# Kernel tuning notes

Hardware: AMD Instinct MI355X
Metric: run time of the kernel (lower is better)

The kernel has to match this reference:

```python
import jax, jax.numpy as jnp
import numpy as np

D_OUT, D_IN, R, N_TOK = 4096, 4096, 16, 8192

def setup_inputs() -> dict:
    key = jax.random.key(0)
    k1, k2, k3, k4 = jax.random.split(key, 4)
    x = jax.random.normal(k1, (N_TOK, D_IN), dtype=jnp.float32)
    W = jax.random.normal(k2, (D_OUT, D_IN), dtype=jnp.float32) * (1.0 / np.sqrt(D_IN))
    bias = jax.random.normal(k3, (D_OUT,), dtype=jnp.float32) * 0.02
    lora_B = jnp.zeros((D_OUT, R), dtype=jnp.float32)  # torch init: zeros
    lora_A = jax.random.normal(k4, (R, D_IN), dtype=jnp.float32) / R  # torch init: randn / r
    lora_scale = jnp.float32(1.0)
    return {"x": x, "W": W, "bias": bias, "lora_B": lora_B, "lora_A": lora_A, "lora_scale": lora_scale}

def reference(x, W, bias, lora_B, lora_A, lora_scale):
    # Faithful to torch: weight = W + scale * B @ A; out = x @ weight.T + bias
    weight = W + lora_scale * (lora_B @ lora_A)  # [d_out, d_in]
    return jnp.einsum('ni,oi->no', x, weight) + bias
```

## Files before the change

kernel.cpp:

```cpp
#include <hip/hip_runtime.h>
#include <stdint.h>
#include <stddef.h>

#define M_TOK 8192
#define N_OUT 4096
#define K_IN  4096
#define R_LORA 16

#define BM 256
#define BN 256
#define BK 64
#define NT (K_IN / BK)

#define WEFF_BLOCKS ((K_IN / 1024) * (N_OUT / 16))
#define CAST_BLOCKS ((M_TOK * K_IN) / (8 * 256))

typedef __bf16 bf16_t;
typedef __bf16 bf16x4 __attribute__((ext_vector_type(4)));
typedef __bf16 bf16x8 __attribute__((ext_vector_type(8)));
typedef float floatx4 __attribute__((ext_vector_type(4)));

__device__ inline void async_copy16(const bf16_t* g, bf16_t* l) {
  __builtin_amdgcn_global_load_lds(
      (__attribute__((address_space(1))) void*)(uintptr_t)(const void*)g,
      (__attribute__((address_space(3))) void*)l,
      16, 0, 0);
}

#define BAR()   __builtin_amdgcn_s_barrier()
#define VMCNT4  asm volatile("s_waitcnt vmcnt(4)" ::: "memory")
#define VMCNT2  asm volatile("s_waitcnt vmcnt(2)" ::: "memory")
#define VMCNT0  asm volatile("s_waitcnt vmcnt(0)" ::: "memory")

__global__ __launch_bounds__(256) void prep_fused(
    const float* __restrict__ x, bf16_t* __restrict__ xb,
    const float* __restrict__ W, const float* __restrict__ lB,
    const float* __restrict__ lA, const float* __restrict__ scale_p,
    bf16_t* __restrict__ wb) {
  const int b = blockIdx.x;
  if (b < WEFF_BLOCKS) {
    const int kbase = (b & 3) * 1024 + threadIdx.x * 4;
    const int o0    = (b >> 2) * 16;
    const float scale = *scale_p;

    float4 areg[R_LORA];
#pragma unroll
    for (int r = 0; r < R_LORA; ++r)
      areg[r] = *(const float4*)(lA + (size_t)r * K_IN + kbase);

    for (int oo = 0; oo < 16; ++oo) {
      const int o = o0 + oo;
      float4 w = *(const float4*)(W + (size_t)o * K_IN + kbase);
      float a0 = w.x, a1 = w.y, a2 = w.z, a3 = w.w;
#pragma unroll
      for (int r = 0; r < R_LORA; ++r) {
        float bb = lB[(size_t)o * R_LORA + r] * scale;
        a0 += bb * areg[r].x; a1 += bb * areg[r].y;
        a2 += bb * areg[r].z; a3 += bb * areg[r].w;
      }
      bf16x4 v;
      v[0] = (bf16_t)a0; v[1] = (bf16_t)a1; v[2] = (bf16_t)a2; v[3] = (bf16_t)a3;
      *(bf16x4*)(wb + (size_t)o * K_IN + kbase) = v;
    }
  } else {
    const size_t t = (size_t)(b - WEFF_BLOCKS) * 256 + threadIdx.x;
    const float4* xp = (const float4*)x + t * 2;
    float4 a0 = xp[0];
    float4 a1 = xp[1];
    bf16x8 v;
    v[0] = (bf16_t)a0.x; v[1] = (bf16_t)a0.y; v[2] = (bf16_t)a0.z; v[3] = (bf16_t)a0.w;
    v[4] = (bf16_t)a1.x; v[5] = (bf16_t)a1.y; v[6] = (bf16_t)a1.z; v[7] = (bf16_t)a1.w;
    *(bf16x8*)(xb + t * 8) = v;
  }
}

__global__ __launch_bounds__(512, 2) void gemm_bt256(const bf16_t* __restrict__ A,
                                                     const bf16_t* __restrict__ Bw,
                                                     const float* __restrict__ bias,
                                                     float* __restrict__ C) {
  __shared__ bf16_t sA[2 * 2 * 128 * 64];
  __shared__ bf16_t sB[2 * 2 * 128 * 64];

  const int tid  = threadIdx.x;
  const int wave = tid >> 6;
  const int lane = tid & 63;
  const int lr   = lane & 15;
  const int quad = lane >> 4;
  const int wr   = wave >> 2;
  const int wc   = wave & 3;

  const int bid = blockIdx.x;
  const int swz = (bid & 7) * 64 + (bid >> 3);
  const int bn  = (swz & 15) * BN;
  const int bm  = (swz >> 4) * BM;

  const int t8  = tid >> 3;
  const int col = ((tid & 7) ^ (t8 & 7)) * 8;
  const bf16_t* pA00 = A + (size_t)(bm +   0 + t8) * K_IN + col;
  const bf16_t* pA01 = A + (size_t)(bm + 128 + t8) * K_IN + col;
  const bf16_t* pA10 = A + (size_t)(bm +  64 + t8) * K_IN + col;
  const bf16_t* pA11 = A + (size_t)(bm + 192 + t8) * K_IN + col;
  const int brl = (t8 >> 5) * 64 + (t8 & 31);
  const bf16_t* pB00 = Bw + (size_t)(bn +   0 + brl +  0) * K_IN + col;
  const bf16_t* pB01 = Bw + (size_t)(bn + 128 + brl +  0) * K_IN + col;
  const bf16_t* pB10 = Bw + (size_t)(bn +   0 + brl + 32) * K_IN + col;
  const bf16_t* pB11 = Bw + (size_t)(bn + 128 + brl + 32) * K_IN + col;

  const char* aR0 = (const char*)sA + (size_t)(wr * 64 + lr) * 128 + ((quad) ^ (lr & 7)) * 16;
  const char* aR1 = (const char*)sA + (size_t)(wr * 64 + lr) * 128 + ((4 + quad) ^ (lr & 7)) * 16;
  const char* bR0 = (const char*)sB + (size_t)(wc * 32 + lr) * 128 + ((quad) ^ (lr & 7)) * 16;
  const char* bR1 = (const char*)sB + (size_t)(wc * 32 + lr) * 128 + ((4 + quad) ^ (lr & 7)) * 16;

  floatx4 acc[8][4];
#pragma unroll
  for (int m = 0; m < 8; ++m)
#pragma unroll
    for (int n = 0; n < 4; ++n) acc[m][n] = {0.f, 0.f, 0.f, 0.f};

  bf16x8 a0[4][2], a1[4][2], bA[2][2], bB[2][2];

#define STAGE_A0(nb) do { \
    async_copy16(pA00, sA + (nb)         + wave * 512); \
    async_copy16(pA01, sA + (nb) + 4096  + wave * 512); \
    pA00 += BK; pA01 += BK; } while (0)
#define STAGE_A1(nb) do { \
    async_copy16(pA10, sA + (nb) + 8192  + wave * 512); \
    async_copy16(pA11, sA + (nb) + 12288 + wave * 512); \
    pA10 += BK; pA11 += BK; } while (0)
#define STAGE_B0(nb) do { \
    async_copy16(pB00, sB + (nb)         + wave * 512); \
    async_copy16(pB01, sB + (nb) + 4096  + wave * 512); \
    pB00 += BK; pB01 += BK; } while (0)
#define STAGE_B1(nb) do { \
    async_copy16(pB10, sB + (nb) + 8192  + wave * 512); \
    async_copy16(pB11, sB + (nb) + 12288 + wave * 512); \
    pB10 += BK; pB11 += BK; } while (0)

#define RD_A(dst, mh, bofs) do { _Pragma("unroll") for (int mm = 0; mm < 4; ++mm) { \
    dst[mm][0] = *(const bf16x8*)(aR0 + (bofs) + (mh) * 16384 + mm * 2048); \
    dst[mm][1] = *(const bf16x8*)(aR1 + (bofs) + (mh) * 16384 + mm * 2048); } } while (0)
#define RD_B(dst, nh, bofs) do { _Pragma("unroll") for (int nn = 0; nn < 2; ++nn) { \
    dst[nn][0] = *(const bf16x8*)(bR0 + (bofs) + (nh) * 16384 + nn * 2048); \
    dst[nn][1] = *(const bf16x8*)(bR1 + (bofs) + (nh) * 16384 + nn * 2048); } } while (0)

#define MM(aset, bset, mh, nh) do { \
    __builtin_amdgcn_s_setprio(1); \
    _Pragma("unroll") for (int mm = 0; mm < 4; ++mm) \
    _Pragma("unroll") for (int nn = 0; nn < 2; ++nn) { \
      acc[(mh)*4+mm][(nh)*2+nn] = __builtin_amdgcn_mfma_f32_16x16x32_bf16( \
          aset[mm][0], bset[nn][0], acc[(mh)*4+mm][(nh)*2+nn], 0, 0, 0); \
      acc[(mh)*4+mm][(nh)*2+nn] = __builtin_amdgcn_mfma_f32_16x16x32_bf16( \
          aset[mm][1], bset[nn][1], acc[(mh)*4+mm][(nh)*2+nn], 0, 0, 0); } \
    __builtin_amdgcn_s_setprio(0); } while (0)

#define TILE(bo, nb, ST) do { \
     \
    RD_A(a0, 0, bo); RD_B(bA, 0, bo); \
    if (ST) { STAGE_A0(nb); VMCNT4; } else { VMCNT2; }    \
    MM(a0, bA, 0, 0); \
    BAR(); \
     \
    RD_B(bB, 1, bo); \
    if (ST) { STAGE_B0(nb); VMCNT4; } else { VMCNT0; }    \
    MM(a0, bB, 0, 1); \
    BAR(); \
     \
    RD_A(a1, 1, bo); \
    if (ST) STAGE_B1(nb);                                 \
    MM(a1, bB, 1, 1); \
    BAR(); \
     \
    if (ST) { STAGE_A1(nb); VMCNT4; }                     \
    MM(a1, bA, 1, 0); \
    BAR(); \
  } while (0)

  STAGE_A0(0); STAGE_B0(0); STAGE_B1(0); STAGE_A1(0);
  VMCNT4;
  BAR();

  for (int t = 0; t < NT - 2; t += 2) {
    TILE(0, 16384, 1);
    TILE(32768, 0, 1);
  }
  TILE(0, 16384, 1);
  TILE(32768, 0, 0);
#undef TILE
#undef STAGE_A0
#undef STAGE_A1
#undef STAGE_B0
#undef STAGE_B1
#undef RD_A
#undef RD_B
#undef MM

#pragma unroll
  for (int n = 0; n < 4; ++n) {
    const int colc = bn + wc * 64 + n * 16 + lr;
    const float bb = bias[colc];
#pragma unroll
    for (int m = 0; m < 8; ++m) {
      const int row0 = bm + wr * 128 + m * 16 + quad * 4;
      floatx4 v = acc[m][n];
#pragma unroll
      for (int r = 0; r < 4; ++r)
        C[(size_t)(row0 + r) * N_OUT + colc] = v[r] + bb;
    }
  }
}

__global__ __launch_bounds__(256) void lora_xa(const float* __restrict__ x,
                                               const float* __restrict__ lA,
                                               const float* __restrict__ scale_p,
                                               float* __restrict__ t) {
  int m = blockIdx.x;
  int r = threadIdx.x & 15;
  int kcn = threadIdx.x >> 4;
  float acc = 0.f;
  const float* xr = x + (size_t)m * K_IN + kcn * 256;
  const float* ar = lA + (size_t)r * K_IN + kcn * 256;
  for (int k = 0; k < 256; k += 4) {
    float4 xv = *(const float4*)(xr + k);
    float4 av = *(const float4*)(ar + k);
    acc += xv.x * av.x + xv.y * av.y + xv.z * av.z + xv.w * av.w;
  }
  __shared__ float s[256];
  s[threadIdx.x] = acc;
  __syncthreads();
  if (threadIdx.x < 16) {
    float v = 0.f;
    for (int i = 0; i < 16; ++i) v += s[threadIdx.x + i * 16];
    t[(size_t)m * 16 + threadIdx.x] = v * (*scale_p);
  }
}

__global__ __launch_bounds__(256) void gemm_f32_fb(const float* __restrict__ X,
                                                   const float* __restrict__ W,
                                                   const float* __restrict__ bias,
                                                   const float* __restrict__ t,
                                                   const float* __restrict__ lB,
                                                   float* __restrict__ C) {
  __shared__ float sX[64][17];
  __shared__ float sW[64][17];
  int tid = threadIdx.x;
  int tx = tid & 15, ty = tid >> 4;
  int m0 = blockIdx.y * 64, n0 = blockIdx.x * 64;
  int lrow = tid >> 2, lcol = (tid & 3) * 4;
  float acc[4][4] = {};
  for (int k0 = 0; k0 < K_IN; k0 += 16) {
    __syncthreads();
    float4 xv = *(const float4*)(X + (size_t)(m0 + lrow) * K_IN + k0 + lcol);
    float4 wv = *(const float4*)(W + (size_t)(n0 + lrow) * K_IN + k0 + lcol);
    sX[lrow][lcol + 0] = xv.x; sX[lrow][lcol + 1] = xv.y;
    sX[lrow][lcol + 2] = xv.z; sX[lrow][lcol + 3] = xv.w;
    sW[lrow][lcol + 0] = wv.x; sW[lrow][lcol + 1] = wv.y;
    sW[lrow][lcol + 2] = wv.z; sW[lrow][lcol + 3] = wv.w;
    __syncthreads();
#pragma unroll
    for (int kk = 0; kk < 16; ++kk) {
      float xr[4], wr[4];
#pragma unroll
      for (int i = 0; i < 4; ++i) { xr[i] = sX[ty * 4 + i][kk]; wr[i] = sW[tx * 4 + i][kk]; }
#pragma unroll
      for (int i = 0; i < 4; ++i)
#pragma unroll
        for (int j = 0; j < 4; ++j) acc[i][j] += xr[i] * wr[j];
    }
  }
  for (int j = 0; j < 4; ++j) {
    int n = n0 + tx * 4 + j;
    float bb = bias[n];
    for (int i = 0; i < 4; ++i) {
      int m = m0 + ty * 4 + i;
      float l = 0.f;
      for (int r = 0; r < R_LORA; ++r) l += t[(size_t)m * 16 + r] * lB[(size_t)n * 16 + r];
      C[(size_t)m * N_OUT + n] = acc[i][j] + bb + l;
    }
  }
}

extern "C" void kernel_launch(void* const* d_in, const int* in_sizes, int n_in,
                              void* d_out, int out_size, void* d_ws, size_t ws_size,
                              hipStream_t stream) {
  const float* x     = (const float*)d_in[0];
  const float* W     = (const float*)d_in[1];
  const float* bias  = (const float*)d_in[2];
  const float* lB    = (const float*)d_in[3];
  const float* lA    = (const float*)d_in[4];
  const float* scale = (const float*)d_in[5];
  float* out = (float*)d_out;

  const size_t x_bytes = (size_t)M_TOK * K_IN * sizeof(bf16_t);
  const size_t w_bytes = (size_t)N_OUT * K_IN * sizeof(bf16_t);

  if (ws_size >= x_bytes + w_bytes) {
    bf16_t* xb = (bf16_t*)d_ws;
    bf16_t* wb = (bf16_t*)((char*)d_ws + x_bytes);
    prep_fused<<<WEFF_BLOCKS + CAST_BLOCKS, 256, 0, stream>>>(x, xb, W, lB, lA, scale, wb);
    gemm_bt256<<<(M_TOK / BM) * (N_OUT / BN), 512, 0, stream>>>(xb, wb, bias, out);
  } else {
    float* t = (float*)d_ws;
    lora_xa<<<M_TOK, 256, 0, stream>>>(x, lA, scale, t);
    gemm_f32_fb<<<dim3(N_OUT / 64, M_TOK / 64), 256, 0, stream>>>(x, W, bias, t, lB, out);
  }
}
```

Before: 518.2 us.

## Deepen async LDS prefetch pipeline by issuing next-tile stages earlier

```diff
diff --git a/kernel.cpp b/kernel.cpp
--- a/kernel.cpp
+++ b/kernel.cpp
@@ -28,6 +28,7 @@
 }
 
 #define BAR()   __builtin_amdgcn_s_barrier()
+#define VMCNT8  asm volatile("s_waitcnt vmcnt(8)" ::: "memory")
 #define VMCNT4  asm volatile("s_waitcnt vmcnt(4)" ::: "memory")
 #define VMCNT2  asm volatile("s_waitcnt vmcnt(2)" ::: "memory")
 #define VMCNT0  asm volatile("s_waitcnt vmcnt(0)" ::: "memory")
@@ -153,38 +154,59 @@
           aset[mm][1], bset[nn][1], acc[(mh)*4+mm][(nh)*2+nn], 0, 0, 0); } \
     __builtin_amdgcn_s_setprio(0); } while (0)
 
-#define TILE(bo, nb, ST) do { \
+#define TILE(bo, eCur, eNxt) do { \
      \
     RD_A(a0, 0, bo); RD_B(bA, 0, bo); \
-    if (ST) { STAGE_A0(nb); VMCNT4; } else { VMCNT2; }    \
+    STAGE_B1(eNxt); VMCNT8;             \
     MM(a0, bA, 0, 0); \
     BAR(); \
      \
     RD_B(bB, 1, bo); \
-    if (ST) { STAGE_B0(nb); VMCNT4; } else { VMCNT0; }    \
+    STAGE_A1(eNxt); VMCNT8;             \
     MM(a0, bB, 0, 1); \
     BAR(); \
      \
     RD_A(a1, 1, bo); \
-    if (ST) STAGE_B1(nb);                                 \
+    STAGE_A0(eCur);                     \
     MM(a1, bB, 1, 1); \
     BAR(); \
      \
-    if (ST) { STAGE_A1(nb); VMCNT4; }                     \
+    STAGE_B0(eCur); VMCNT8;             \
     MM(a1, bA, 1, 0); \
     BAR(); \
   } while (0)
 
-  STAGE_A0(0); STAGE_B0(0); STAGE_B1(0); STAGE_A1(0);
+  STAGE_A0(0); STAGE_B0(0);
+  STAGE_B1(0); STAGE_A1(0);
+  STAGE_A0(16384); STAGE_B0(16384);
+  VMCNT8;
+  BAR();
+
+  for (int t = 0; t < NT - 2; t += 2) {
+    TILE(0, 0, 16384);
+    TILE(32768, 16384, 0);
+  }
+
+  RD_A(a0, 0, 0); RD_B(bA, 0, 0);
+  STAGE_B1(16384); VMCNT8;
+  MM(a0, bA, 0, 0); BAR();
+  RD_B(bB, 1, 0);
+  STAGE_A1(16384); VMCNT8;
+  MM(a0, bB, 0, 1); BAR();
+  RD_A(a1, 1, 0);
+  MM(a1, bB, 1, 1); BAR();
   VMCNT4;
-  BAR();
-
-  for (int t = 0; t < NT - 2; t += 2) {
-    TILE(0, 16384, 1);
-    TILE(32768, 0, 1);
-  }
-  TILE(0, 16384, 1);
-  TILE(32768, 0, 0);
+  MM(a1, bA, 1, 0); BAR();
+
+  RD_A(a0, 0, 32768); RD_B(bA, 0, 32768);
+  VMCNT2;
+  MM(a0, bA, 0, 0); BAR();
+  RD_B(bB, 1, 32768);
+  VMCNT0;
+  MM(a0, bB, 0, 1); BAR();
+  RD_A(a1, 1, 32768);
+  MM(a1, bB, 1, 1); BAR();
+  MM(a1, bA, 1, 0); BAR();
 #undef TILE
 #undef STAGE_A0
 #undef STAGE_A1
```

New measurement: 498.7 us. -3.8%, faster.
